# Optimization experiments

Hardware: AMD Instinct MI355X
Metric: run time of the kernel (lower is better)

Reference implementation:

```python
import jax, jax.numpy as jnp
import numpy as np


def setup_inputs() -> dict:
    key = jax.random.key(0)
    k1, k2, k3 = jax.random.split(key, 3)
    B, S, H = 64, 2048, 1024
    return {
        "dec_state_h": jax.random.normal(k1, (B, H), dtype=jnp.float32),
        "dec_state_c": jax.random.normal(k2, (B, H), dtype=jnp.float32),
        "enc_output": jax.random.normal(k3, (B, S, H), dtype=jnp.float32),
    }


def reference(dec_state_h, dec_state_c, enc_output):
    # dec_state: [B, H] = h + c  (Luong-style combined decoder state)
    dec_state = dec_state_h + dec_state_c
    # score[b, s] = sum_h enc_output[b, s, h] * dec_state[b, h]  -> [B, S, 1]
    score = jnp.einsum("bsh,bh->bs", enc_output, dec_state)[..., None]
    # softmax over the sequence axis
    attention_weights = jax.nn.softmax(score, axis=1)  # [B, S, 1]
    # context[b, h] = sum_s attn[b, s] * enc_output[b, s, h]
    context_vector = jnp.einsum("bs,bsh->bh", attention_weights[..., 0], enc_output)
    return context_vector, attention_weights
```

## Files before the change

### kernel.cpp

```cpp
#include <hip/hip_runtime.h>
#include <math.h>

#define B 64
#define S 2048
#define H 1024
#define SPLIT 16
#define ROWS_PER_BLOCK (S / SPLIT)
#define THREADS 256
#define WAVES 4
#define ROWS_PER_WAVE (ROWS_PER_BLOCK / WAVES)

__global__ __launch_bounds__(THREADS, 4)
void luong_pass1(const float* __restrict__ dec_h,
                 const float* __restrict__ dec_c,
                 const float* __restrict__ enc,
                 float* __restrict__ attn_raw,
                 float* __restrict__ ctx_part,
                 float* __restrict__ mz_part) {
  const int bid  = blockIdx.x;
  const int b    = bid / SPLIT;
  const int sp   = bid % SPLIT;
  const int t    = threadIdx.x;
  const int w    = t >> 6;
  const int lane = t & 63;

  float4 dec[4];
  const float4* dh = (const float4*)(dec_h + (size_t)b * H);
  const float4* dc = (const float4*)(dec_c + (size_t)b * H);
#pragma unroll
  for (int c = 0; c < 4; ++c) {
    float4 a  = dh[c * 64 + lane];
    float4 bb = dc[c * 64 + lane];
    dec[c] = make_float4(a.x + bb.x, a.y + bb.y, a.z + bb.z, a.w + bb.w);
  }

  float m = -INFINITY;
  float Z = 0.f;
  float ctx[16];
#pragma unroll
  for (int k = 0; k < 16; ++k) ctx[k] = 0.f;

  const int s_base = sp * ROWS_PER_BLOCK + w;
  const float4* ebase = (const float4*)(enc + ((size_t)b * S + s_base) * H);

  float4 buf[3][4];

#define LOADR(SL, R) do {                                                      \
    const float4* rp_ = ebase + (size_t)(R) * (WAVES * (H / 4));               \
    _Pragma("unroll")                                                          \
    for (int c_ = 0; c_ < 4; ++c_) buf[SL][c_] = rp_[c_ * 64 + lane];          \
  } while (0)

#define PROCR(SL, R) do {                                                      \
    float p_ = 0.f;                                                            \
    _Pragma("unroll")                                                          \
    for (int c_ = 0; c_ < 4; ++c_)                                             \
      p_ += buf[SL][c_].x * dec[c_].x + buf[SL][c_].y * dec[c_].y +            \
            buf[SL][c_].z * dec[c_].z + buf[SL][c_].w * dec[c_].w;             \
    _Pragma("unroll")                                                          \
    for (int off_ = 32; off_ >= 1; off_ >>= 1)                                 \
      p_ += __shfl_xor(p_, off_, 64);                                          \
    if (lane == 0) attn_raw[b * S + s_base + (R) * WAVES] = p_;                \
    if (p_ > m) {                                                              \
      const float f_ = expf(m - p_);                                           \
      Z *= f_;                                                                 \
      _Pragma("unroll")                                                        \
      for (int k_ = 0; k_ < 16; ++k_) ctx[k_] *= f_;                           \
      m = p_;                                                                  \
    }                                                                          \
    const float e_ = expf(p_ - m);                                             \
    Z += e_;                                                                   \
    _Pragma("unroll")                                                          \
    for (int c_ = 0; c_ < 4; ++c_) {                                           \
      ctx[c_ * 4 + 0] += e_ * buf[SL][c_].x;                                   \
      ctx[c_ * 4 + 1] += e_ * buf[SL][c_].y;                                   \
      ctx[c_ * 4 + 2] += e_ * buf[SL][c_].z;                                   \
      ctx[c_ * 4 + 3] += e_ * buf[SL][c_].w;                                   \
    }                                                                          \
  } while (0)

  LOADR(0, 0);
  LOADR(1, 1);
  for (int i = 0; i < ROWS_PER_WAVE - 2; i += 3) {
    LOADR(2, i + 2);
    PROCR(0, i);
    LOADR(0, i + 3);
    PROCR(1, i + 1);
    LOADR(1, i + 4);
    PROCR(2, i + 2);
  }
  PROCR(0, ROWS_PER_WAVE - 2);
  PROCR(1, ROWS_PER_WAVE - 1);

#undef LOADR
#undef PROCR

  __shared__ float ctx_lds[WAVES][H];
  __shared__ float mzs[WAVES][2];
#pragma unroll
  for (int c = 0; c < 4; ++c) {
    float4 v = make_float4(ctx[c * 4 + 0], ctx[c * 4 + 1],
                           ctx[c * 4 + 2], ctx[c * 4 + 3]);
    ((float4*)&ctx_lds[w][c * 256])[lane] = v;
  }
  if (lane == 0) { mzs[w][0] = m; mzs[w][1] = Z; }
  __syncthreads();

  const float M = fmaxf(fmaxf(mzs[0][0], mzs[1][0]),
                        fmaxf(mzs[2][0], mzs[3][0]));
  float fac[WAVES];
  float Zb = 0.f;
#pragma unroll
  for (int i = 0; i < WAVES; ++i) {
    fac[i] = expf(mzs[i][0] - M);
    Zb += mzs[i][1] * fac[i];
  }

  float* outp = ctx_part + ((size_t)b * SPLIT + sp) * H;
#pragma unroll
  for (int q = 0; q < 4; ++q) {
    const int h = q * 256 + t;
    float v = 0.f;
#pragma unroll
    for (int i = 0; i < WAVES; ++i) v += ctx_lds[i][h] * fac[i];
    outp[h] = v;
  }
  if (t == 0) {
    mz_part[(b * SPLIT + sp) * 2 + 0] = M;
    mz_part[(b * SPLIT + sp) * 2 + 1] = Zb;
  }
}

__global__ __launch_bounds__(256)
void luong_combine(const float* __restrict__ ctx_part,
                   const float* __restrict__ mz_part,
                   float* __restrict__ ctx_out,
                   float* __restrict__ mz_final) {
  const int b = blockIdx.x;
  const int t = threadIdx.x;

  float m_i[SPLIT], z_i[SPLIT];
  float M = -INFINITY;
#pragma unroll
  for (int i = 0; i < SPLIT; ++i) {
    m_i[i] = mz_part[(b * SPLIT + i) * 2 + 0];
    z_i[i] = mz_part[(b * SPLIT + i) * 2 + 1];
    M = fmaxf(M, m_i[i]);
  }
  float fac[SPLIT];
  float Z = 0.f;
#pragma unroll
  for (int i = 0; i < SPLIT; ++i) {
    fac[i] = expf(m_i[i] - M);
    Z += z_i[i] * fac[i];
  }
  const float invZ = 1.f / Z;

#pragma unroll
  for (int q = 0; q < 4; ++q) {
    const int h = q * 256 + t;
    float v = 0.f;
#pragma unroll
    for (int i = 0; i < SPLIT; ++i)
      v += ctx_part[((size_t)(b * SPLIT + i)) * H + h] * fac[i];
    ctx_out[(size_t)b * H + h] = v * invZ;
  }
  if (t == 0) {
    mz_final[2 * b + 0] = M;
    mz_final[2 * b + 1] = Z;
  }
}

__global__ __launch_bounds__(256)
void luong_fixup(float* __restrict__ attn,
                 const float* __restrict__ mz_final) {
  const int idx = blockIdx.x * blockDim.x + threadIdx.x;
  if (idx >= B * S) return;
  const int b = idx >> 11;
  const float M = mz_final[2 * b + 0];
  const float Z = mz_final[2 * b + 1];
  attn[idx] = expf(attn[idx] - M) / Z;
}

extern "C" void kernel_launch(void* const* d_in, const int* in_sizes, int n_in,
                              void* d_out, int out_size, void* d_ws, size_t ws_size,
                              hipStream_t stream) {
  const float* dec_h = (const float*)d_in[0];
  const float* dec_c = (const float*)d_in[1];
  const float* enc   = (const float*)d_in[2];

  float* ctx_out = (float*)d_out;
  float* attn    = (float*)d_out + B * H;

  float* ctx_part = (float*)d_ws;
  float* mz_part  = ctx_part + (size_t)B * SPLIT * H;
  float* mz_final = mz_part + (size_t)B * SPLIT * 2;

  luong_pass1<<<B * SPLIT, THREADS, 0, stream>>>(dec_h, dec_c, enc, attn,
                                                 ctx_part, mz_part);
  luong_combine<<<B, 256, 0, stream>>>(ctx_part, mz_part, ctx_out, mz_final);
  luong_fixup<<<(B * S + 255) / 256, 256, 0, stream>>>(attn, mz_final);
}
```

Before: 116.1 us.

## Fuse combine and softmax fixup, template split count and raise grid parallelism

Merges the combine and attention-fixup kernels into one tail kernel spread over four blocks per batch, which removes one launch and the mz_final round-trip. The split count becomes a template parameter and is raised to 32 when the workspace allows, doubling the pass-1 grid for better occupancy. The pass-1 loop drops from a triple buffer to a fully unrolled double buffer, and the occupancy hint goes from 4 to 5. The trade-off is a shallower prefetch depth per wave and more partial context vectors for the tail kernel to read.

```diff
diff --git a/kernel.cpp b/kernel.cpp
--- a/kernel.cpp
+++ b/kernel.cpp
@@ -4,19 +4,20 @@
 #define B 64
 #define S 2048
 #define H 1024
-#define SPLIT 16
-#define ROWS_PER_BLOCK (S / SPLIT)
 #define THREADS 256
 #define WAVES 4
-#define ROWS_PER_WAVE (ROWS_PER_BLOCK / WAVES)
 
-__global__ __launch_bounds__(THREADS, 4)
+template <int SPLIT>
+__global__ __launch_bounds__(THREADS, 5)
 void luong_pass1(const float* __restrict__ dec_h,
                  const float* __restrict__ dec_c,
                  const float* __restrict__ enc,
                  float* __restrict__ attn_raw,
                  float* __restrict__ ctx_part,
                  float* __restrict__ mz_part) {
+  constexpr int ROWS_PER_BLOCK = S / SPLIT;
+  constexpr int RPW = ROWS_PER_BLOCK / WAVES;
+
   const int bid  = blockIdx.x;
   const int b    = bid / SPLIT;
   const int sp   = bid % SPLIT;
@@ -43,7 +44,7 @@
   const int s_base = sp * ROWS_PER_BLOCK + w;
   const float4* ebase = (const float4*)(enc + ((size_t)b * S + s_base) * H);
 
-  float4 buf[3][4];
+  float4 buf[2][4];
 
 #define LOADR(SL, R) do {                                                      \
     const float4* rp_ = ebase + (size_t)(R) * (WAVES * (H / 4));               \
@@ -80,17 +81,13 @@
   } while (0)
 
   LOADR(0, 0);
-  LOADR(1, 1);
-  for (int i = 0; i < ROWS_PER_WAVE - 2; i += 3) {
-    LOADR(2, i + 2);
+#pragma unroll
+  for (int i = 0; i < RPW; i += 2) {
+    if (i + 1 < RPW) LOADR(1, i + 1);
     PROCR(0, i);
-    LOADR(0, i + 3);
-    PROCR(1, i + 1);
-    LOADR(1, i + 4);
-    PROCR(2, i + 2);
+    if (i + 2 < RPW) LOADR(0, i + 2);
+    if (i + 1 < RPW) PROCR(1, i + 1);
   }
-  PROCR(0, ROWS_PER_WAVE - 2);
-  PROCR(1, ROWS_PER_WAVE - 1);
 
 #undef LOADR
 #undef PROCR
@@ -131,55 +128,56 @@
   }
 }
 
+template <int SPLIT>
 __global__ __launch_bounds__(256)
-void luong_combine(const float* __restrict__ ctx_part,
-                   const float* __restrict__ mz_part,
-                   float* __restrict__ ctx_out,
-                   float* __restrict__ mz_final) {
-  const int b = blockIdx.x;
-  const int t = threadIdx.x;
+void luong_tail(const float* __restrict__ ctx_part,
+                const float* __restrict__ mz_part,
+                float* __restrict__ ctx_out,
+                float* __restrict__ attn) {
+  const int b  = blockIdx.x >> 2;
+  const int q4 = blockIdx.x & 3;
+  const int t  = threadIdx.x;
 
-  float m_i[SPLIT], z_i[SPLIT];
+  const float* mz = mz_part + (size_t)b * SPLIT * 2;
+
   float M = -INFINITY;
 #pragma unroll
-  for (int i = 0; i < SPLIT; ++i) {
-    m_i[i] = mz_part[(b * SPLIT + i) * 2 + 0];
-    z_i[i] = mz_part[(b * SPLIT + i) * 2 + 1];
-    M = fmaxf(M, m_i[i]);
-  }
-  float fac[SPLIT];
+  for (int i = 0; i < SPLIT; ++i) M = fmaxf(M, mz[2 * i]);
   float Z = 0.f;
 #pragma unroll
-  for (int i = 0; i < SPLIT; ++i) {
-    fac[i] = expf(m_i[i] - M);
-    Z += z_i[i] * fac[i];
-  }
+  for (int i = 0; i < SPLIT; ++i) Z += mz[2 * i + 1] * expf(mz[2 * i] - M);
   const float invZ = 1.f / Z;
 
-#pragma unroll
-  for (int q = 0; q < 4; ++q) {
-    const int h = q * 256 + t;
+  __shared__ float fac_s[SPLIT];
+  if (t < SPLIT) fac_s[t] = expf(mz[2 * t] - M);
+  __syncthreads();
+
+  {
+    const int h = q4 * 256 + t;
     float v = 0.f;
 #pragma unroll
     for (int i = 0; i < SPLIT; ++i)
-      v += ctx_part[((size_t)(b * SPLIT + i)) * H + h] * fac[i];
+      v += ctx_part[((size_t)b * SPLIT + i) * H + h] * fac_s[i];
     ctx_out[(size_t)b * H + h] = v * invZ;
   }
-  if (t == 0) {
-    mz_final[2 * b + 0] = M;
-    mz_final[2 * b + 1] = Z;
+
+#pragma unroll
+  for (int k = 0; k < 2; ++k) {
+    const int s = q4 * 512 + k * 256 + t;
+    const size_t idx = (size_t)b * S + s;
+    attn[idx] = expf(attn[idx] - M) * invZ;
   }
 }
 
-__global__ __launch_bounds__(256)
-void luong_fixup(float* __restrict__ attn,
-                 const float* __restrict__ mz_final) {
-  const int idx = blockIdx.x * blockDim.x + threadIdx.x;
-  if (idx >= B * S) return;
-  const int b = idx >> 11;
-  const float M = mz_final[2 * b + 0];
-  const float Z = mz_final[2 * b + 1];
-  attn[idx] = expf(attn[idx] - M) / Z;
+template <int SPLIT>
+static void launch_all(const float* dec_h, const float* dec_c, const float* enc,
+                       float* ctx_out, float* attn, void* d_ws,
+                       hipStream_t stream) {
+  float* ctx_part = (float*)d_ws;
+  float* mz_part  = ctx_part + (size_t)B * SPLIT * H;
+  luong_pass1<SPLIT><<<B * SPLIT, THREADS, 0, stream>>>(dec_h, dec_c, enc,
+                                                        attn, ctx_part, mz_part);
+  luong_tail<SPLIT><<<B * 4, 256, 0, stream>>>(ctx_part, mz_part, ctx_out, attn);
 }
 
 extern "C" void kernel_launch(void* const* d_in, const int* in_sizes, int n_in,
@@ -192,12 +190,10 @@
   float* ctx_out = (float*)d_out;
   float* attn    = (float*)d_out + B * H;
 
-  float* ctx_part = (float*)d_ws;
-  float* mz_part  = ctx_part + (size_t)B * SPLIT * H;
-  float* mz_final = mz_part + (size_t)B * SPLIT * 2;
-
-  luong_pass1<<<B * SPLIT, THREADS, 0, stream>>>(dec_h, dec_c, enc, attn,
-                                                 ctx_part, mz_part);
-  luong_combine<<<B, 256, 0, stream>>>(ctx_part, mz_part, ctx_out, mz_final);
-  luong_fixup<<<(B * S + 255) / 256, 256, 0, stream>>>(attn, mz_final);
+  const size_t need32 = ((size_t)B * 32 * H + (size_t)B * 32 * 2) * sizeof(float);
+  if (ws_size >= need32) {
+    launch_all<32>(dec_h, dec_c, enc, ctx_out, attn, d_ws, stream);
+  } else {
+    launch_all<16>(dec_h, dec_c, enc, ctx_out, attn, d_ws, stream);
+  }
 }
```

Result: slower. 141.2 us (+21.6%).
